# Kernel tuning notes

Measured on AMD Instinct MI355X. Metric: run time of the kernel, lower is better.

The kernel has to match this reference:

```python
import jax, jax.numpy as jnp
import numpy as np

SIZE = (48, 48, 48)          # (D, H, W)
C = 125
CP = C + 3                   # conv channels = 128
N_KPTS = 512
EPS = 1e-5                   # InstanceNorm3d default eps


def make_grid(size):
    # torch affine_grid(identity, align_corners=True): last dim is (x, y, z),
    # x varies along W, y along H, z along D, each in [-1, 1].
    D, H, W = size
    zs = jnp.linspace(-1.0, 1.0, D)
    ys = jnp.linspace(-1.0, 1.0, H)
    xs = jnp.linspace(-1.0, 1.0, W)
    gz, gy, gx = jnp.meshgrid(zs, ys, xs, indexing='ij')
    return jnp.stack([gx, gy, gz], axis=0)[None]  # (1, 3, D, H, W) == grid.permute(0,4,1,2,3)


def conv3d(x, w, b):
    # Conv3d(kernel=3, stride=1, pad=1) == SAME
    y = jax.lax.conv_general_dilated(
        x, w, window_strides=(1, 1, 1), padding='SAME',
        dimension_numbers=('NCDHW', 'OIDHW', 'NCDHW'))
    return y + b.reshape(1, -1, 1, 1, 1)


def instance_norm(x):
    # InstanceNorm3d(affine=False): per-(batch, channel) normalization over D,H,W
    mu = jnp.mean(x, axis=(2, 3, 4), keepdims=True)
    var = jnp.mean((x - mu) ** 2, axis=(2, 3, 4), keepdims=True)
    return (x - mu) * jax.lax.rsqrt(var + EPS)


def grid_sample_points(vol, pts):
    # vol: (C, D, H, W); pts: (N, 3) as (x, y, z) in [-1, 1]
    # trilinear, align_corners=True (points assumed in-range, so index clamping is exact)
    Cc, D, H, W = vol.shape
    ix = (pts[:, 0] + 1.0) * 0.5 * (W - 1)
    iy = (pts[:, 1] + 1.0) * 0.5 * (H - 1)
    iz = (pts[:, 2] + 1.0) * 0.5 * (D - 1)
    x0f, y0f, z0f = jnp.floor(ix), jnp.floor(iy), jnp.floor(iz)
    wx, wy, wz = ix - x0f, iy - y0f, iz - z0f
    x0 = jnp.clip(x0f.astype(jnp.int32), 0, W - 1)
    y0 = jnp.clip(y0f.astype(jnp.int32), 0, H - 1)
    z0 = jnp.clip(z0f.astype(jnp.int32), 0, D - 1)
    x1 = jnp.clip(x0 + 1, 0, W - 1)
    y1 = jnp.clip(y0 + 1, 0, H - 1)
    z1 = jnp.clip(z0 + 1, 0, D - 1)

    def g(zi, yi, xi):
        return vol[:, zi, yi, xi]  # (C, N)

    out = (g(z0, y0, x0) * ((1 - wz) * (1 - wy) * (1 - wx))
         + g(z0, y0, x1) * ((1 - wz) * (1 - wy) * wx)
         + g(z0, y1, x0) * ((1 - wz) * wy * (1 - wx))
         + g(z0, y1, x1) * ((1 - wz) * wy * wx)
         + g(z1, y0, x0) * (wz * (1 - wy) * (1 - wx))
         + g(z1, y0, x1) * (wz * (1 - wy) * wx)
         + g(z1, y1, x0) * (wz * wy * (1 - wx))
         + g(z1, y1, x1) * (wz * wy * wx))
    return out  # (C, N)


def setup_inputs() -> dict:
    key = jax.random.key(0)
    k1, k2, k3, k4 = jax.random.split(key, 4)
    kpts = jax.random.uniform(k1, (1, N_KPTS, 3), dtype=jnp.float32,
                              minval=-0.95, maxval=0.95)
    disp = jax.random.normal(k2, (1, N_KPTS, 3), dtype=jnp.float32) * 0.1
    feats = jax.random.normal(k3, (1, C) + SIZE, dtype=jnp.float32)
    W0 = jax.random.normal(k4, (CP, CP, 3, 3, 3), dtype=jnp.float32) * (1.0 / np.sqrt(CP * 27))
    b0 = jnp.zeros((CP,), dtype=jnp.float32)
    return {"kpts": kpts, "disp": disp, "feats": feats, "W0": W0, "b0": b0}


def reference(kpts, disp, feats, W0, b0):
    B = feats.shape[0]
    grid = make_grid(SIZE)                                   # (1, 3, D, H, W)
    fg = jnp.concatenate([feats, jnp.broadcast_to(grid, (B, 3) + SIZE)], axis=1)
    fg = instance_norm(jax.nn.relu(conv3d(fg, W0, b0)))      # (B, CP, D, H, W)

    fk = jax.vmap(grid_sample_points)(fg, kpts)              # (B, CP, N)
    fgf = fg.reshape(B, CP, -1)                              # (B, CP, Ng)

    # ||f_g - f_n||^2 via Gram expansion (avoids (B,CP,Ng,N) intermediate)
    cross = jnp.einsum('bcg,bcn->bgn', fgf, fk)              # (B, Ng, N)
    d2 = (jnp.sum(fgf ** 2, axis=1)[:, :, None]
          + jnp.sum(fk ** 2, axis=1)[:, None, :]
          - 2.0 * cross)
    # exp(-d2) / sum_n exp(-d2) == softmax(-d2) over keypoints (stable form)
    K = jax.nn.softmax(-d2, axis=2)                          # (B, Ng, N)

    disp_grid = jnp.einsum('bgn,bnd->bgd', K, disp)          # (B, Ng, 3)
    disp_grid = disp_grid.reshape((1,) + SIZE + (3,)).transpose(0, 4, 1, 2, 3)
    return disp_grid                                         # (1, 3, D, H, W)
```

## Files before the change

### kernel.cpp

```cpp
#include <hip/hip_runtime.h>
#include <math.h>

#define NG 110592
#define NCH 128
#define NKP 512
#define EPSN 1e-5f

typedef _Float16 half8 __attribute__((ext_vector_type(8)));
typedef float floatx4 __attribute__((ext_vector_type(4)));
typedef unsigned short ushort_t;

static __device__ __forceinline__ ushort_t h2u(_Float16 h) {
    union { _Float16 f; ushort_t u; } x; x.f = h; return x.u;
}

__global__ __launch_bounds__(256) void k_prep_w(const float* __restrict__ W0,
                                                ushort_t* __restrict__ Wp) {
    int idx = blockIdx.x * 256 + threadIdx.x;
    int s   = idx >> 13;
    int rem = idx & 8191;
    int h   = rem >> 12;
    int r3  = rem & 4095;
    int co  = r3 >> 5;
    int cip = r3 & 31;
    int cc  = s / 27, tap = s - cc * 27;
    int ci  = cc * 32 + cip;
    float w = W0[co * 3456 + ci * 27 + tap];
    _Float16 hi = (_Float16)w;
    Wp[idx] = (h == 0) ? h2u(hi) : h2u((_Float16)(w - (float)hi));
}

__global__ __launch_bounds__(256) void k_cvt(const float* __restrict__ feats,
                                             ushort_t* __restrict__ f16) {
    int idx = blockIdx.x * 256 + threadIdx.x;
    int cc  = idx / NG;
    int vox = idx - cc * NG;
    int gx = vox % 48, gy = (vox / 48) % 48, gz = vox / 2304;
    const float sc = 2.0f / 47.0f;
    ushort_t* dst = f16 + (size_t)idx * 32;
    #pragma unroll
    for (int o = 0; o < 4; ++o) {
        half8 h;
        #pragma unroll
        for (int j = 0; j < 8; ++j) {
            int ci = cc * 32 + o * 8 + j;
            float v = (ci < 125) ? feats[(size_t)ci * NG + vox]
                                 : ((ci == 125 ? gx : (ci == 126 ? gy : gz)) * sc - 1.0f);
            h[j] = (_Float16)v;
        }
        *(half8*)(dst + o * 8) = h;
    }
}

__global__ __launch_bounds__(128, 2) void k_conv(const ushort_t* __restrict__ f16,
                                                 const ushort_t* __restrict__ Wp,
                                                 const float* __restrict__ b0,
                                                 float* __restrict__ yout,
                                                 float* __restrict__ gsum,
                                                 float* __restrict__ gsq) {
    __shared__ __align__(16) ushort_t hA0[14400];
    __shared__ float lsum[128], lsq[128];

    const int tid = threadIdx.x;
    const int blk = blockIdx.x;
    const int bz = blk / 72, by = (blk % 72) / 6, bx = blk % 6;
    const int z0 = bz * 4, y0v = by * 4, x0 = bx * 8;

    const int wave = tid >> 6, lane = tid & 63;
    const int ll = lane & 15, kq = lane >> 4;
    const int chalf = wave * 64;

    lsum[tid] = 0.f; lsq[tid] = 0.f;

    int abase[8];
    #pragma unroll
    for (int mi = 0; mi < 8; ++mi) {
        int v = mi * 16 + ll;
        int vz = v >> 5, vy = (v >> 3) & 3, vx = v & 7;
        abase[mi] = (vz * 60 + vy * 10 + vx) * 80 + kq * 16;
    }
    int idxh[4];
    #pragma unroll
    for (int ni = 0; ni < 4; ++ni)
        idxh[ni] = (chalf + ni * 16 + ll) * 4 + kq;

    floatx4 acc[8][4];
    const floatx4 zz = {0.f, 0.f, 0.f, 0.f};
    #pragma unroll
    for (int mi = 0; mi < 8; ++mi)
        #pragma unroll
        for (int ni = 0; ni < 4; ++ni) acc[mi][ni] = zz;

    half8 Bh[4];
    {
        const half8* bp = (const half8*)Wp;
        #pragma unroll
        for (int ni = 0; ni < 4; ++ni) Bh[ni] = bp[idxh[ni]];
    }

    for (int cc = 0; cc < 4; ++cc) {
        __syncthreads();
        for (int u = tid; u < 1440; u += 128) {
            int pos = u >> 2, c8 = u & 3;
            int zi = pos / 60, rem = pos - zi * 60;
            int yi = rem / 10, xi = rem - yi * 10;
            int gz = z0 - 1 + zi, gy = y0v - 1 + yi, gx = x0 - 1 + xi;
            bool inb = ((unsigned)gz < 48u) & ((unsigned)gy < 48u) & ((unsigned)gx < 48u);
            half8 h;
            #pragma unroll
            for (int j = 0; j < 8; ++j) h[j] = (_Float16)0.f;
            if (inb) {
                size_t off = ((size_t)(cc * NG + gz * 2304 + gy * 48 + gx)) * 32 + c8 * 8;
                h = *(const half8*)(f16 + off);
            }
            *(half8*)(&hA0[pos * 40 + c8 * 8]) = h;
        }
        __syncthreads();

        for (int tap = 0; tap < 27; ++tap) {
            const int it = cc * 27 + tap;
            int itn = it + 1; if (itn > 107) itn = 107;
            const half8* bpn = (const half8*)(Wp + (size_t)itn * 8192);
            half8 Bhn[4];
            #pragma unroll
            for (int ni = 0; ni < 4; ++ni) Bhn[ni] = bpn[idxh[ni]];

            const int tb = (tap / 9) * 4800 + ((tap / 3) % 3) * 800 + (tap % 3) * 80;
            half8 Ah[8];
            #pragma unroll
            for (int mi = 0; mi < 8; ++mi)
                Ah[mi] = *(const half8*)((const char*)hA0 + (abase[mi] + tb));

            #pragma unroll
            for (int mi = 0; mi < 8; ++mi)
                #pragma unroll
                for (int ni = 0; ni < 4; ++ni)
                    acc[mi][ni] = __builtin_amdgcn_mfma_f32_16x16x32_f16(Ah[mi], Bh[ni], acc[mi][ni], 0, 0, 0);

            #pragma unroll
            for (int ni = 0; ni < 4; ++ni) Bh[ni] = Bhn[ni];
        }
    }

    #pragma unroll
    for (int ni = 0; ni < 4; ++ni) {
        int co = chalf + ni * 16 + ll;
        float b = b0[co];
        float s = 0.f, q = 0.f;
        #pragma unroll
        for (int mi = 0; mi < 8; ++mi) {
            #pragma unroll
            for (int r = 0; r < 4; ++r) {
                int v = mi * 16 + kq * 4 + r;
                int vz = v >> 5, vy = (v >> 3) & 3, vx = v & 7;
                float val = acc[mi][ni][r] + b;
                val = val > 0.f ? val : 0.f;
                yout[(size_t)co * NG + (z0 + vz) * 2304 + (y0v + vy) * 48 + (x0 + vx)] = val;
                s += val; q += val * val;
            }
        }
        atomicAdd(&lsum[co], s);
        atomicAdd(&lsq[co], q);
    }
    __syncthreads();
    if (wave == 0) {
        atomicAdd(&gsum[tid + 0],  lsum[tid + 0]);
        atomicAdd(&gsq[tid + 0],   lsq[tid + 0]);
        atomicAdd(&gsum[tid + 64], lsum[tid + 64]);
        atomicAdd(&gsq[tid + 64],  lsq[tid + 64]);
    }
}

__global__ void k_finalize(const float* __restrict__ gsum, const float* __restrict__ gsq,
                           float* __restrict__ mu, float* __restrict__ inv) {
    int c = threadIdx.x;
    float m = gsum[c] * (1.0f / NG);
    float v = gsq[c] * (1.0f / NG) - m * m;
    mu[c] = m;
    inv[c] = rsqrtf(v + EPSN);
}

__global__ __launch_bounds__(128) void k_sample(const float* __restrict__ kpts,
                                                const float* __restrict__ yin,
                                                const float* __restrict__ mu,
                                                const float* __restrict__ inv,
                                                ushort_t* __restrict__ fkH,
                                                float* __restrict__ fkn2) {
    __shared__ float red[128];
    const int n = blockIdx.x, c = threadIdx.x;
    float px = kpts[n * 3 + 0], py = kpts[n * 3 + 1], pz = kpts[n * 3 + 2];
    float ix = (px + 1.f) * 0.5f * 47.f;
    float iy = (py + 1.f) * 0.5f * 47.f;
    float iz = (pz + 1.f) * 0.5f * 47.f;
    float xf = floorf(ix), yf = floorf(iy), zf = floorf(iz);
    float wx = ix - xf, wy = iy - yf, wz = iz - zf;
    int x0 = min(max((int)xf, 0), 47), y0 = min(max((int)yf, 0), 47), z0 = min(max((int)zf, 0), 47);
    int x1 = min(x0 + 1, 47), y1 = min(y0 + 1, 47), z1 = min(z0 + 1, 47);

    const float* base = yin + (size_t)c * NG;
    float v000 = base[z0 * 2304 + y0 * 48 + x0];
    float v001 = base[z0 * 2304 + y0 * 48 + x1];
    float v010 = base[z0 * 2304 + y1 * 48 + x0];
    float v011 = base[z0 * 2304 + y1 * 48 + x1];
    float v100 = base[z1 * 2304 + y0 * 48 + x0];
    float v101 = base[z1 * 2304 + y0 * 48 + x1];
    float v110 = base[z1 * 2304 + y1 * 48 + x0];
    float v111 = base[z1 * 2304 + y1 * 48 + x1];

    float val = v000 * (1 - wz) * (1 - wy) * (1 - wx)
              + v001 * (1 - wz) * (1 - wy) * wx
              + v010 * (1 - wz) * wy * (1 - wx)
              + v011 * (1 - wz) * wy * wx
              + v100 * wz * (1 - wy) * (1 - wx)
              + v101 * wz * (1 - wy) * wx
              + v110 * wz * wy * (1 - wx)
              + v111 * wz * wy * wx;

    val = (val - mu[c]) * inv[c];
    fkH[n * 128 + c] = h2u((_Float16)val);
    red[c] = val * val;
    __syncthreads();
    for (int s = 64; s > 0; s >>= 1) {
        if (c < s) red[c] += red[c + s];
        __syncthreads();
    }
    if (c == 0) fkn2[n] = red[0];
}

__global__ __launch_bounds__(256, 2) void k_attn(const float* __restrict__ yb,
                                                 const float* __restrict__ mu,
                                                 const float* __restrict__ inv,
                                                 const ushort_t* __restrict__ fkH,
                                                 const float* __restrict__ fk2,
                                                 const float* __restrict__ disp,
                                                 float* __restrict__ out) {
    __shared__ __align__(16) ushort_t fgH[64 * 136];
    __shared__ __align__(16) ushort_t fgL[64 * 136];
    __shared__ float dspx[512], dspy[512], dspz[512];
    __shared__ float fk2s[512];
    __shared__ float mrg[64 * 4 * 5];

    const int tid = threadIdx.x;
    const int gbase = blockIdx.x * 64;
    const int wave = tid >> 6, lane = tid & 63;
    const int ll = lane & 15, kq = lane >> 4;

    {
        int v = tid & 63;
        int c0 = (tid >> 6) * 32;
        #pragma unroll
        for (int o = 0; o < 4; ++o) {
            half8 h, l;
            #pragma unroll
            for (int j = 0; j < 8; ++j) {
                int c = c0 + o * 8 + j;
                float x = yb[(size_t)c * NG + gbase + v];
                x = (x - mu[c]) * inv[c];
                _Float16 hh = (_Float16)x;
                h[j] = hh;
                l[j] = (_Float16)(x - (float)hh);
            }
            *(half8*)&fgH[v * 136 + c0 + o * 8] = h;
            *(half8*)&fgL[v * 136 + c0 + o * 8] = l;
        }
    }
    for (int s = tid; s < 512; s += 256) {
        dspx[s] = disp[3 * s + 0];
        dspy[s] = disp[3 * s + 1];
        dspz[s] = disp[3 * s + 2];
        fk2s[s] = fk2[s];
    }
    __syncthreads();

    const int key0 = wave * 128;

    floatx4 acc[8][4];
    const floatx4 zz = {0.f, 0.f, 0.f, 0.f};
    #pragma unroll
    for (int mi = 0; mi < 8; ++mi)
        #pragma unroll
        for (int ni = 0; ni < 4; ++ni) acc[mi][ni] = zz;

    #pragma unroll
    for (int ks = 0; ks < 4; ++ks) {
        half8 Bh[4], Bl[4];
        #pragma unroll
        for (int ni = 0; ni < 4; ++ni) {
            int ad = (ni * 16 + ll) * 136 + ks * 32 + kq * 8;
            Bh[ni] = *(const half8*)&fgH[ad];
            Bl[ni] = *(const half8*)&fgL[ad];
        }
        #pragma unroll
        for (int mi = 0; mi < 8; ++mi) {
            int key = key0 + mi * 16 + ll;
            int ga = key * 128 + ks * 32 + kq * 8;
            half8 Ah = *(const half8*)&fkH[ga];
            #pragma unroll
            for (int ni = 0; ni < 4; ++ni) {
                acc[mi][ni] = __builtin_amdgcn_mfma_f32_16x16x32_f16(Ah, Bh[ni], acc[mi][ni], 0, 0, 0);
                acc[mi][ni] = __builtin_amdgcn_mfma_f32_16x16x32_f16(Ah, Bl[ni], acc[mi][ni], 0, 0, 0);
            }
        }
    }

    float mx[4] = {-1e30f, -1e30f, -1e30f, -1e30f};
    #pragma unroll
    for (int mi = 0; mi < 8; ++mi)
        #pragma unroll
        for (int r = 0; r < 4; ++r) {
            int key = key0 + mi * 16 + kq * 4 + r;
            float f2 = fk2s[key];
            #pragma unroll
            for (int ni = 0; ni < 4; ++ni) {
                float s = 2.f * acc[mi][ni][r] - f2;
                acc[mi][ni][r] = s;
                mx[ni] = fmaxf(mx[ni], s);
            }
        }
    #pragma unroll
    for (int ni = 0; ni < 4; ++ni) {
        mx[ni] = fmaxf(mx[ni], __shfl_xor(mx[ni], 16, 64));
        mx[ni] = fmaxf(mx[ni], __shfl_xor(mx[ni], 32, 64));
    }

    float lv[4] = {0.f, 0.f, 0.f, 0.f};
    float pxv[4] = {0.f, 0.f, 0.f, 0.f};
    float pyv[4] = {0.f, 0.f, 0.f, 0.f};
    float pzv[4] = {0.f, 0.f, 0.f, 0.f};
    #pragma unroll
    for (int mi = 0; mi < 8; ++mi)
        #pragma unroll
        for (int r = 0; r < 4; ++r) {
            int key = key0 + mi * 16 + kq * 4 + r;
            float dx = dspx[key], dy = dspy[key], dz = dspz[key];
            #pragma unroll
            for (int ni = 0; ni < 4; ++ni) {
                float p = __expf(acc[mi][ni][r] - mx[ni]);
                lv[ni] += p;
                pxv[ni] = fmaf(p, dx, pxv[ni]);
                pyv[ni] = fmaf(p, dy, pyv[ni]);
                pzv[ni] = fmaf(p, dz, pzv[ni]);
            }
        }
    #pragma unroll
    for (int ni = 0; ni < 4; ++ni) {
        lv[ni]  += __shfl_xor(lv[ni], 16, 64);  lv[ni]  += __shfl_xor(lv[ni], 32, 64);
        pxv[ni] += __shfl_xor(pxv[ni], 16, 64); pxv[ni] += __shfl_xor(pxv[ni], 32, 64);
        pyv[ni] += __shfl_xor(pyv[ni], 16, 64); pyv[ni] += __shfl_xor(pyv[ni], 32, 64);
        pzv[ni] += __shfl_xor(pzv[ni], 16, 64); pzv[ni] += __shfl_xor(pzv[ni], 32, 64);
    }

    if (kq == 0) {
        #pragma unroll
        for (int ni = 0; ni < 4; ++ni) {
            int vox = ni * 16 + ll;
            float* q = &mrg[(vox * 4 + wave) * 5];
            q[0] = mx[ni]; q[1] = lv[ni]; q[2] = pxv[ni]; q[3] = pyv[ni]; q[4] = pzv[ni];
        }
    }
    __syncthreads();

    if (tid < 64) {
        float M = -1e30f;
        #pragma unroll
        for (int w = 0; w < 4; ++w) M = fmaxf(M, mrg[(tid * 4 + w) * 5]);
        float L = 0.f, X = 0.f, Y = 0.f, Z = 0.f;
        #pragma unroll
        for (int w = 0; w < 4; ++w) {
            const float* q = &mrg[(tid * 4 + w) * 5];
            float a = __expf(q[0] - M);
            L = fmaf(q[1], a, L);
            X = fmaf(q[2], a, X);
            Y = fmaf(q[3], a, Y);
            Z = fmaf(q[4], a, Z);
        }
        float il = 1.0f / L;
        out[0 * NG + gbase + tid] = X * il;
        out[1 * NG + gbase + tid] = Y * il;
        out[2 * NG + gbase + tid] = Z * il;
    }
}

extern "C" void kernel_launch(void* const* d_in, const int* in_sizes, int n_in,
                              void* d_out, int out_size, void* d_ws, size_t ws_size,
                              hipStream_t stream) {
    const float* kpts  = (const float*)d_in[0];
    const float* disp  = (const float*)d_in[1];
    const float* feats = (const float*)d_in[2];
    const float* W0    = (const float*)d_in[3];
    const float* b0    = (const float*)d_in[4];

    float* ws = (float*)d_ws;
    float*    yb   = ws;
    ushort_t* Wp   = (ushort_t*)(yb + (size_t)NCH * NG);
    float*    gsum = yb + (size_t)NCH * NG + 442368;
    float*    gsq  = gsum + 128;
    float*    mu   = gsq + 128;
    float*    ivr  = mu + 128;
    float*    fk2  = ivr + 128;
    ushort_t* fkH  = (ushort_t*)(fk2 + 512);
    ushort_t* f16  = fkH + 65536;

    k_prep_w<<<3456, 256, 0, stream>>>(W0, Wp);
    k_cvt<<<1728, 256, 0, stream>>>(feats, f16);
    hipMemsetAsync(gsum, 0, 256 * sizeof(float), stream);
    k_conv<<<864, 128, 0, stream>>>(f16, Wp, b0, yb, gsum, gsq);
    k_finalize<<<1, 128, 0, stream>>>(gsum, gsq, mu, ivr);
    k_sample<<<NKP, 128, 0, stream>>>(kpts, yb, mu, ivr, fkH, fk2);
    k_attn<<<1728, 256, 0, stream>>>(yb, mu, ivr, fkH, fk2, disp, (float*)d_out);
}
```

Baseline: 279.5 us.

## Enlarge conv tile to 8x4x8 voxels with 4 waves and fuse prep kernels

The conv kernel now uses 256-thread blocks covering 8x4x8 voxels. Each wave computes 32 output channels across all 256 voxels, so the fp16 halo tile loaded into shared memory is reused by more output voxels and costs less load per voxel. The next-tap weight prefetch into registers is dropped, and weights are now loaded at the start of each tap. The weight-packing and feature-conversion kernels are merged into one launch. The risks are that 432 blocks fill the CUs less evenly than the old 864, and that the larger accumulator and A-fragment arrays raise register pressure and can stall on weight loads.

```diff
diff --git a/kernel.cpp b/kernel.cpp
--- a/kernel.cpp
+++ b/kernel.cpp
@@ -14,93 +14,88 @@
     union { _Float16 f; ushort_t u; } x; x.f = h; return x.u;
 }
 
-__global__ __launch_bounds__(256) void k_prep_w(const float* __restrict__ W0,
-                                                ushort_t* __restrict__ Wp) {
-    int idx = blockIdx.x * 256 + threadIdx.x;
-    int s   = idx >> 13;
-    int rem = idx & 8191;
-    int h   = rem >> 12;
-    int r3  = rem & 4095;
-    int co  = r3 >> 5;
-    int cip = r3 & 31;
-    int cc  = s / 27, tap = s - cc * 27;
-    int ci  = cc * 32 + cip;
-    float w = W0[co * 3456 + ci * 27 + tap];
-    _Float16 hi = (_Float16)w;
-    Wp[idx] = (h == 0) ? h2u(hi) : h2u((_Float16)(w - (float)hi));
-}
-
-__global__ __launch_bounds__(256) void k_cvt(const float* __restrict__ feats,
-                                             ushort_t* __restrict__ f16) {
-    int idx = blockIdx.x * 256 + threadIdx.x;
-    int cc  = idx / NG;
-    int vox = idx - cc * NG;
-    int gx = vox % 48, gy = (vox / 48) % 48, gz = vox / 2304;
-    const float sc = 2.0f / 47.0f;
-    ushort_t* dst = f16 + (size_t)idx * 32;
-    #pragma unroll
-    for (int o = 0; o < 4; ++o) {
-        half8 h;
-        #pragma unroll
-        for (int j = 0; j < 8; ++j) {
-            int ci = cc * 32 + o * 8 + j;
-            float v = (ci < 125) ? feats[(size_t)ci * NG + vox]
-                                 : ((ci == 125 ? gx : (ci == 126 ? gy : gz)) * sc - 1.0f);
-            h[j] = (_Float16)v;
-        }
-        *(half8*)(dst + o * 8) = h;
-    }
-}
-
-__global__ __launch_bounds__(128, 2) void k_conv(const ushort_t* __restrict__ f16,
+__global__ __launch_bounds__(256) void k_prep(const float* __restrict__ W0,
+                                              ushort_t* __restrict__ Wp,
+                                              const float* __restrict__ feats,
+                                              ushort_t* __restrict__ f16) {
+    int b = blockIdx.x;
+    if (b < 3456) {
+        int idx = b * 256 + threadIdx.x;
+        int s   = idx >> 13;
+        int rem = idx & 8191;
+        int h   = rem >> 12;
+        int r3  = rem & 4095;
+        int co  = r3 >> 5;
+        int cip = r3 & 31;
+        int cc  = s / 27, tap = s - cc * 27;
+        int ci  = cc * 32 + cip;
+        float w = W0[co * 3456 + ci * 27 + tap];
+        _Float16 hi = (_Float16)w;
+        Wp[idx] = (h == 0) ? h2u(hi) : h2u((_Float16)(w - (float)hi));
+    } else {
+        int idx = (b - 3456) * 256 + threadIdx.x;
+        int cc  = idx / NG;
+        int vox = idx - cc * NG;
+        int gx = vox % 48, gy = (vox / 48) % 48, gz = vox / 2304;
+        const float sc = 2.0f / 47.0f;
+        ushort_t* dst = f16 + (size_t)idx * 32;
+        #pragma unroll
+        for (int o = 0; o < 4; ++o) {
+            half8 h;
+            #pragma unroll
+            for (int j = 0; j < 8; ++j) {
+                int ci = cc * 32 + o * 8 + j;
+                float v = (ci < 125) ? feats[(size_t)ci * NG + vox]
+                                     : ((ci == 125 ? gx : (ci == 126 ? gy : gz)) * sc - 1.0f);
+                h[j] = (_Float16)v;
+            }
+            *(half8*)(dst + o * 8) = h;
+        }
+    }
+}
+
+__global__ __launch_bounds__(256, 2) void k_conv(const ushort_t* __restrict__ f16,
                                                  const ushort_t* __restrict__ Wp,
                                                  const float* __restrict__ b0,
                                                  float* __restrict__ yout,
                                                  float* __restrict__ gsum,
                                                  float* __restrict__ gsq) {
-    __shared__ __align__(16) ushort_t hA0[14400];
+    __shared__ __align__(16) ushort_t hA0[24000];
     __shared__ float lsum[128], lsq[128];
 
     const int tid = threadIdx.x;
     const int blk = blockIdx.x;
     const int bz = blk / 72, by = (blk % 72) / 6, bx = blk % 6;
-    const int z0 = bz * 4, y0v = by * 4, x0 = bx * 8;
+    const int z0 = bz * 8, y0v = by * 4, x0 = bx * 8;
 
     const int wave = tid >> 6, lane = tid & 63;
     const int ll = lane & 15, kq = lane >> 4;
-    const int chalf = wave * 64;
-
-    lsum[tid] = 0.f; lsq[tid] = 0.f;
-
-    int abase[8];
-    #pragma unroll
-    for (int mi = 0; mi < 8; ++mi) {
+    const int c32 = wave * 32;
+
+    if (tid < 128) { lsum[tid] = 0.f; lsq[tid] = 0.f; }
+
+    int abase[16];
+    #pragma unroll
+    for (int mi = 0; mi < 16; ++mi) {
         int v = mi * 16 + ll;
         int vz = v >> 5, vy = (v >> 3) & 3, vx = v & 7;
         abase[mi] = (vz * 60 + vy * 10 + vx) * 80 + kq * 16;
     }
-    int idxh[4];
-    #pragma unroll
-    for (int ni = 0; ni < 4; ++ni)
-        idxh[ni] = (chalf + ni * 16 + ll) * 4 + kq;
-
-    floatx4 acc[8][4];
+    int idxh[2];
+    #pragma unroll
+    for (int ni = 0; ni < 2; ++ni)
+        idxh[ni] = (c32 + ni * 16 + ll) * 4 + kq;
+
+    floatx4 acc[16][2];
     const floatx4 zz = {0.f, 0.f, 0.f, 0.f};
     #pragma unroll
-    for (int mi = 0; mi < 8; ++mi)
-        #pragma unroll
-        for (int ni = 0; ni < 4; ++ni) acc[mi][ni] = zz;
-
-    half8 Bh[4];
-    {
-        const half8* bp = (const half8*)Wp;
-        #pragma unroll
-        for (int ni = 0; ni < 4; ++ni) Bh[ni] = bp[idxh[ni]];
-    }
+    for (int mi = 0; mi < 16; ++mi)
+        #pragma unroll
+        for (int ni = 0; ni < 2; ++ni) acc[mi][ni] = zz;
 
     for (int cc = 0; cc < 4; ++cc) {
         __syncthreads();
-        for (int u = tid; u < 1440; u += 128) {
+        for (int u = tid; u < 2400; u += 256) {
             int pos = u >> 2, c8 = u & 3;
             int zi = pos / 60, rem = pos - zi * 60;
             int yi = rem / 10, xi = rem - yi * 10;
@@ -119,36 +114,33 @@
 
         for (int tap = 0; tap < 27; ++tap) {
             const int it = cc * 27 + tap;
-            int itn = it + 1; if (itn > 107) itn = 107;
-            const half8* bpn = (const half8*)(Wp + (size_t)itn * 8192);
-            half8 Bhn[4];
-            #pragma unroll
-            for (int ni = 0; ni < 4; ++ni) Bhn[ni] = bpn[idxh[ni]];
+            const half8* bp = (const half8*)(Wp + (size_t)it * 8192);
+
+            half8 Bh[2];
+            #pragma unroll
+            for (int ni = 0; ni < 2; ++ni) Bh[ni] = bp[idxh[ni]];
 
             const int tb = (tap / 9) * 4800 + ((tap / 3) % 3) * 800 + (tap % 3) * 80;
-            half8 Ah[8];
-            #pragma unroll
-            for (int mi = 0; mi < 8; ++mi)
+            half8 Ah[16];
+            #pragma unroll
+            for (int mi = 0; mi < 16; ++mi)
                 Ah[mi] = *(const half8*)((const char*)hA0 + (abase[mi] + tb));
 
             #pragma unroll
-            for (int mi = 0; mi < 8; ++mi)
+            for (int mi = 0; mi < 16; ++mi)
                 #pragma unroll
-                for (int ni = 0; ni < 4; ++ni)
+                for (int ni = 0; ni < 2; ++ni)
                     acc[mi][ni] = __builtin_amdgcn_mfma_f32_16x16x32_f16(Ah[mi], Bh[ni], acc[mi][ni], 0, 0, 0);
-
-            #pragma unroll
-            for (int ni = 0; ni < 4; ++ni) Bh[ni] = Bhn[ni];
-        }
-    }
-
-    #pragma unroll
-    for (int ni = 0; ni < 4; ++ni) {
-        int co = chalf + ni * 16 + ll;
+        }
+    }
+
+    #pragma unroll
+    for (int ni = 0; ni < 2; ++ni) {
+        int co = c32 + ni * 16 + ll;
         float b = b0[co];
         float s = 0.f, q = 0.f;
         #pragma unroll
-        for (int mi = 0; mi < 8; ++mi) {
+        for (int mi = 0; mi < 16; ++mi) {
             #pragma unroll
             for (int r = 0; r < 4; ++r) {
                 int v = mi * 16 + kq * 4 + r;
@@ -163,12 +155,7 @@
         atomicAdd(&lsq[co], q);
     }
     __syncthreads();
-    if (wave == 0) {
-        atomicAdd(&gsum[tid + 0],  lsum[tid + 0]);
-        atomicAdd(&gsq[tid + 0],   lsq[tid + 0]);
-        atomicAdd(&gsum[tid + 64], lsum[tid + 64]);
-        atomicAdd(&gsq[tid + 64],  lsq[tid + 64]);
-    }
+    if (tid < 128) { atomicAdd(&gsum[tid], lsum[tid]); atomicAdd(&gsq[tid], lsq[tid]); }
 }
 
 __global__ void k_finalize(const float* __restrict__ gsum, const float* __restrict__ gsq,
@@ -401,10 +388,9 @@
     ushort_t* fkH  = (ushort_t*)(fk2 + 512);
     ushort_t* f16  = fkH + 65536;
 
-    k_prep_w<<<3456, 256, 0, stream>>>(W0, Wp);
-    k_cvt<<<1728, 256, 0, stream>>>(feats, f16);
+    k_prep<<<5184, 256, 0, stream>>>(W0, Wp, feats, f16);
     hipMemsetAsync(gsum, 0, 256 * sizeof(float), stream);
-    k_conv<<<864, 128, 0, stream>>>(f16, Wp, b0, yb, gsum, gsq);
+    k_conv<<<432, 256, 0, stream>>>(f16, Wp, b0, yb, gsum, gsq);
     k_finalize<<<1, 128, 0, stream>>>(gsum, gsq, mu, ivr);
     k_sample<<<NKP, 128, 0, stream>>>(kpts, yb, mu, ivr, fkH, fk2);
     k_attn<<<1728, 256, 0, stream>>>(yb, mu, ivr, fkH, fk2, disp, (float*)d_out);
```

Result: slower. 300.8 us (+7.6%).
